# Performance work log

Measured on AMD Instinct MI355X. Metric: run time of the kernel, lower is better.

The kernel has to match this reference:

```python
import jax, jax.numpy as jnp
import numpy as np

EPS = 1.0


def _onedirectional_dist(a, b):
    # a: (B, M), b: (B, N) -> per-batch sum over M of min_n (a_m - b_n)^2
    d2 = (a[:, :, None] - b[:, None, :]) ** 2  # (B, M, N)
    return jnp.min(d2, axis=2).sum(axis=1)  # (B,)


def setup_inputs() -> dict:
    key = jax.random.key(0)
    k1, k2, k3 = jax.random.split(key, 3)
    target = jax.random.uniform(k1, (4, 240, 320), dtype=jnp.float32)
    bin_centers = jax.random.uniform(k2, (4, 256), dtype=jnp.float32)
    mask = jax.random.randint(k3, (4, 240, 320), 0, 2).astype(jnp.bool_)
    return {"target": target, "bin_centers": bin_centers, "mask": mask}


def reference(target, bin_centers, mask):
    # masked path of ChamferDistanceLoss.forward
    max_target = jnp.max(jnp.where(mask, target, -jnp.inf))
    max_center = jnp.max(bin_centers)
    mx = jnp.maximum(max_target, max_center)
    mn = jnp.minimum(max_target, max_center)
    pad_value = mx + (mx - mn) + EPS
    B = bin_centers.shape[0]
    # pad bin_centers with one extra column = pad_value
    mod_centers = jnp.concatenate(
        [bin_centers, jnp.broadcast_to(pad_value, (B, 1)).astype(bin_centers.dtype)],
        axis=1,
    )  # (B, n_bins + 1)
    # invalid target pixels replaced by pad_value
    mod_target = jnp.where(mask, target, pad_value).reshape(B, -1)  # (B, H*W)
    bidir = _onedirectional_dist(mod_centers, mod_target) + _onedirectional_dist(
        mod_target, mod_centers
    )
    return jnp.mean(bidir)
```

## Files before the change

### kernel.cpp

```cpp
#include <hip/hip_runtime.h>
#include <math.h>

#define B 4
#define HW 76800
#define NBINS 256
#define TPB 256
#define PXB 256
#define BPB (HW / PXB)


__global__ __launch_bounds__(256) void kmain(const float* __restrict__ target,
                                             const int* __restrict__ mask,
                                             const float* __restrict__ centers,
                                             float* __restrict__ out,
                                             float* __restrict__ part) {
    __shared__ __align__(16) float s_p[PXB];
    __shared__ __align__(16) float s_c[NBINS];
    __shared__ __align__(16) float s_c2[NBINS];
    __shared__ __align__(16) float s_d1[4][NBINS];
    __shared__ float s_red[4];
    const int tid = threadIdx.x;
    const int b   = blockIdx.y;
    const int blk = blockIdx.x;

    const int base = b * HW + blk * PXB;
    const float p = target[base + tid];
    const int   m = mask[base + tid];
    const float pm = m ? p : 1e18f;
    s_p[tid] = pm;
    {
        const float c = centers[b * NBINS + tid];
        s_c[tid]  = c;
        s_c2[tid] = c * c;
    }
    __syncthreads();

    const float q = p + p;
    float mnA = INFINITY, mnB = INFINITY;
    const float4* c4  = (const float4*)s_c;
    const float4* c24 = (const float4*)s_c2;
#pragma unroll 4
    for (int g = 0; g < NBINS / 8; ++g) {
        float4 ca = c4[2 * g],  cb = c4[2 * g + 1];
        float4 xa = c24[2 * g], xb = c24[2 * g + 1];
        float a0 = fmaf(-ca.x, q, xa.x), a1 = fmaf(-ca.y, q, xa.y);
        float a2 = fmaf(-ca.z, q, xa.z), a3 = fmaf(-ca.w, q, xa.w);
        mnA = fminf(mnA, fminf(fminf(a0, a1), fminf(a2, a3)));
        float b0 = fmaf(-cb.x, q, xb.x), b1 = fmaf(-cb.y, q, xb.y);
        float b2 = fmaf(-cb.z, q, xb.z), b3 = fmaf(-cb.w, q, xb.w);
        mnB = fminf(mnB, fminf(fminf(b0, b1), fminf(b2, b3)));
    }
    float acc = m ? fmaf(p, p, fminf(mnA, mnB)) : 0.f;

    const int w = tid >> 6, lane = tid & 63;
    const float4 cv = ((const float4*)s_c)[lane];
    float mk0 = INFINITY, mk1 = INFINITY, mk2 = INFINITY, mk3 = INFINITY;
    const float4* p4 = (const float4*)s_p;
#pragma unroll 8
    for (int j = 0; j < PXB / 4 / 4; ++j) {
        float4 pp = p4[w * 16 + j];
        float qx = pp.x + pp.x, sx = pp.x * pp.x;
        float qy = pp.y + pp.y, sy = pp.y * pp.y;
        float qz = pp.z + pp.z, sz = pp.z * pp.z;
        float qw = pp.w + pp.w, sw = pp.w * pp.w;
        float d0 = fmaf(-cv.x, qx, sx), d1 = fmaf(-cv.x, qy, sy);
        float d2 = fmaf(-cv.x, qz, sz), d3 = fmaf(-cv.x, qw, sw);
        mk0 = fminf(mk0, fminf(fminf(d0, d1), fminf(d2, d3)));
        float e0 = fmaf(-cv.y, qx, sx), e1 = fmaf(-cv.y, qy, sy);
        float e2 = fmaf(-cv.y, qz, sz), e3 = fmaf(-cv.y, qw, sw);
        mk1 = fminf(mk1, fminf(fminf(e0, e1), fminf(e2, e3)));
        float f0 = fmaf(-cv.z, qx, sx), f1 = fmaf(-cv.z, qy, sy);
        float f2 = fmaf(-cv.z, qz, sz), f3 = fmaf(-cv.z, qw, sw);
        mk2 = fminf(mk2, fminf(fminf(f0, f1), fminf(f2, f3)));
        float g0 = fmaf(-cv.w, qx, sx), g1 = fmaf(-cv.w, qy, sy);
        float g2 = fmaf(-cv.w, qz, sz), g3 = fmaf(-cv.w, qw, sw);
        mk3 = fminf(mk3, fminf(fminf(g0, g1), fminf(g2, g3)));
    }
    ((float4*)s_d1[w])[lane] = make_float4(mk0, mk1, mk2, mk3);

    for (int o = 32; o > 0; o >>= 1) acc += __shfl_down(acc, o);
    if (lane == 0) s_red[w] = acc;
    __syncthreads();

    float v = fminf(fminf(s_d1[0][tid], s_d1[1][tid]),
                    fminf(s_d1[2][tid], s_d1[3][tid]));
    part[(b * BPB + blk) * NBINS + tid] = v;

    if (tid == 0)
        atomicAdd(out, 0.25f * (s_red[0] + s_red[1] + s_red[2] + s_red[3]));
}

__global__ __launch_bounds__(256) void kfold(const float* __restrict__ centers,
                                             const float* __restrict__ part,
                                             float* __restrict__ out) {
    __shared__ float s_red[4];
    const int tid = threadIdx.x;
    const int b   = blockIdx.x;
    const float* pp = part + b * (BPB * NBINS) + tid;
    float m0 = INFINITY, m1 = INFINITY, m2 = INFINITY, m3 = INFINITY;
#pragma unroll 5
    for (int k = 0; k < BPB / 4; ++k) {
        m0 = fminf(m0, pp[(4 * k + 0) * NBINS]);
        m1 = fminf(m1, pp[(4 * k + 1) * NBINS]);
        m2 = fminf(m2, pp[(4 * k + 2) * NBINS]);
        m3 = fminf(m3, pp[(4 * k + 3) * NBINS]);
    }
    const float c = centers[b * NBINS + tid];
    float sum = fminf(fminf(m0, m1), fminf(m2, m3)) + c * c;
    for (int o = 32; o > 0; o >>= 1) sum += __shfl_down(sum, o);
    if ((tid & 63) == 0) s_red[tid >> 6] = sum;
    __syncthreads();
    if (tid == 0)
        atomicAdd(out, 0.25f * (s_red[0] + s_red[1] + s_red[2] + s_red[3]));
}

extern "C" void kernel_launch(void* const* d_in, const int* in_sizes, int n_in,
                              void* d_out, int out_size, void* d_ws, size_t ws_size,
                              hipStream_t stream) {
    const float* target  = (const float*)d_in[0];
    const float* centers = (const float*)d_in[1];
    const int*   mask    = (const int*)d_in[2];
    float* out  = (float*)d_out;
    float* part = (float*)d_ws;

    dim3 g(BPB, B);
    kmain<<<g, TPB, 0, stream>>>(target, mask, centers, out, part);
    kfold<<<dim3(B), TPB, 0, stream>>>(centers, part, out);
}
```

Baseline: 83.66 us.

## Drop LDS staging in main kernel and parallelize fold across bin groups

The main kernel no longer stages pixels and centers in shared memory with a barrier. It reads centers straight from global memory (uniform scalar loads) and re-reads target and mask per wave inside the center-side loop. The pixel-side min now uses the direct (c-p)^2 form instead of the expanded c^2-2cp form. The fold kernel is spread over 16 bin-groups per batch rather than one block per batch, giving more parallelism for the reduction of partial minima at the cost of more atomics.

```diff
diff --git a/kernel.cpp b/kernel.cpp
--- a/kernel.cpp
+++ b/kernel.cpp
@@ -7,6 +7,7 @@
 #define TPB 256
 #define PXB 256
 #define BPB (HW / PXB)
+#define FOLD_CB 16
 
 
 __global__ __launch_bounds__(256) void kmain(const float* __restrict__ target,
@@ -14,67 +15,54 @@
                                              const float* __restrict__ centers,
                                              float* __restrict__ out,
                                              float* __restrict__ part) {
-    __shared__ __align__(16) float s_p[PXB];
-    __shared__ __align__(16) float s_c[NBINS];
-    __shared__ __align__(16) float s_c2[NBINS];
     __shared__ __align__(16) float s_d1[4][NBINS];
     __shared__ float s_red[4];
-    const int tid = threadIdx.x;
-    const int b   = blockIdx.y;
-    const int blk = blockIdx.x;
+    const int tid  = threadIdx.x;
+    const int b    = blockIdx.y;
+    const int blk  = blockIdx.x;
+    const int lane = tid & 63;
+    const int w    = tid >> 6;
+    const int base = b * HW + blk * PXB;
 
-    const int base = b * HW + blk * PXB;
     const float p = target[base + tid];
     const int   m = mask[base + tid];
-    const float pm = m ? p : 1e18f;
-    s_p[tid] = pm;
-    {
-        const float c = centers[b * NBINS + tid];
-        s_c[tid]  = c;
-        s_c2[tid] = c * c;
-    }
-    __syncthreads();
+    const float4 cv = ((const float4*)(centers + b * NBINS))[lane];
 
-    const float q = p + p;
+    const float* __restrict__ cb = centers + b * NBINS;
     float mnA = INFINITY, mnB = INFINITY;
-    const float4* c4  = (const float4*)s_c;
-    const float4* c24 = (const float4*)s_c2;
 #pragma unroll 4
     for (int g = 0; g < NBINS / 8; ++g) {
-        float4 ca = c4[2 * g],  cb = c4[2 * g + 1];
-        float4 xa = c24[2 * g], xb = c24[2 * g + 1];
-        float a0 = fmaf(-ca.x, q, xa.x), a1 = fmaf(-ca.y, q, xa.y);
-        float a2 = fmaf(-ca.z, q, xa.z), a3 = fmaf(-ca.w, q, xa.w);
-        mnA = fminf(mnA, fminf(fminf(a0, a1), fminf(a2, a3)));
-        float b0 = fmaf(-cb.x, q, xb.x), b1 = fmaf(-cb.y, q, xb.y);
-        float b2 = fmaf(-cb.z, q, xb.z), b3 = fmaf(-cb.w, q, xb.w);
-        mnB = fminf(mnB, fminf(fminf(b0, b1), fminf(b2, b3)));
+        const float c0 = cb[8 * g + 0], c1 = cb[8 * g + 1];
+        const float c2 = cb[8 * g + 2], c3 = cb[8 * g + 3];
+        const float c4 = cb[8 * g + 4], c5 = cb[8 * g + 5];
+        const float c6 = cb[8 * g + 6], c7 = cb[8 * g + 7];
+        float t0 = c0 - p, t1 = c1 - p, t2 = c2 - p, t3 = c3 - p;
+        float t4 = c4 - p, t5 = c5 - p, t6 = c6 - p, t7 = c7 - p;
+        float d0 = t0 * t0, d1 = t1 * t1, d2 = t2 * t2, d3 = t3 * t3;
+        float d4 = t4 * t4, d5 = t5 * t5, d6 = t6 * t6, d7 = t7 * t7;
+        mnA = fminf(fminf(mnA, d3), fminf(fminf(d0, d1), d2));
+        mnB = fminf(fminf(mnB, d7), fminf(fminf(d4, d5), d6));
     }
-    float acc = m ? fmaf(p, p, fminf(mnA, mnB)) : 0.f;
+    float acc = m ? fminf(mnA, mnB) : 0.f;
 
-    const int w = tid >> 6, lane = tid & 63;
-    const float4 cv = ((const float4*)s_c)[lane];
+    const int wbase = base + __builtin_amdgcn_readfirstlane(w << 6);
     float mk0 = INFINITY, mk1 = INFINITY, mk2 = INFINITY, mk3 = INFINITY;
-    const float4* p4 = (const float4*)s_p;
-#pragma unroll 8
-    for (int j = 0; j < PXB / 4 / 4; ++j) {
-        float4 pp = p4[w * 16 + j];
-        float qx = pp.x + pp.x, sx = pp.x * pp.x;
-        float qy = pp.y + pp.y, sy = pp.y * pp.y;
-        float qz = pp.z + pp.z, sz = pp.z * pp.z;
-        float qw = pp.w + pp.w, sw = pp.w * pp.w;
-        float d0 = fmaf(-cv.x, qx, sx), d1 = fmaf(-cv.x, qy, sy);
-        float d2 = fmaf(-cv.x, qz, sz), d3 = fmaf(-cv.x, qw, sw);
-        mk0 = fminf(mk0, fminf(fminf(d0, d1), fminf(d2, d3)));
-        float e0 = fmaf(-cv.y, qx, sx), e1 = fmaf(-cv.y, qy, sy);
-        float e2 = fmaf(-cv.y, qz, sz), e3 = fmaf(-cv.y, qw, sw);
-        mk1 = fminf(mk1, fminf(fminf(e0, e1), fminf(e2, e3)));
-        float f0 = fmaf(-cv.z, qx, sx), f1 = fmaf(-cv.z, qy, sy);
-        float f2 = fmaf(-cv.z, qz, sz), f3 = fmaf(-cv.z, qw, sw);
-        mk2 = fminf(mk2, fminf(fminf(f0, f1), fminf(f2, f3)));
-        float g0 = fmaf(-cv.w, qx, sx), g1 = fmaf(-cv.w, qy, sy);
-        float g2 = fmaf(-cv.w, qz, sz), g3 = fmaf(-cv.w, qw, sw);
-        mk3 = fminf(mk3, fminf(fminf(g0, g1), fminf(g2, g3)));
+#pragma unroll 4
+    for (int j = 0; j < 64; j += 2) {
+        const float pa = target[wbase + j], pb = target[wbase + j + 1];
+        const int   ma = mask[wbase + j],   mb = mask[wbase + j + 1];
+        const float va = ma ? pa : 1e18f;
+        const float vb = mb ? pb : 1e18f;
+        float qa = va + va, sa = va * va;
+        float qb = vb + vb, sb = vb * vb;
+        float d0a = fmaf(-cv.x, qa, sa), d0b = fmaf(-cv.x, qb, sb);
+        float d1a = fmaf(-cv.y, qa, sa), d1b = fmaf(-cv.y, qb, sb);
+        float d2a = fmaf(-cv.z, qa, sa), d2b = fmaf(-cv.z, qb, sb);
+        float d3a = fmaf(-cv.w, qa, sa), d3b = fmaf(-cv.w, qb, sb);
+        mk0 = fminf(fminf(mk0, d0a), d0b);
+        mk1 = fminf(fminf(mk1, d1a), d1b);
+        mk2 = fminf(fminf(mk2, d2a), d2b);
+        mk3 = fminf(fminf(mk3, d3a), d3b);
     }
     ((float4*)s_d1[w])[lane] = make_float4(mk0, mk1, mk2, mk3);
 
@@ -93,25 +81,27 @@
 __global__ __launch_bounds__(256) void kfold(const float* __restrict__ centers,
                                              const float* __restrict__ part,
                                              float* __restrict__ out) {
-    __shared__ float s_red[4];
+    __shared__ float s_m[16][FOLD_CB];
     const int tid = threadIdx.x;
-    const int b   = blockIdx.x;
-    const float* pp = part + b * (BPB * NBINS) + tid;
-    float m0 = INFINITY, m1 = INFINITY, m2 = INFINITY, m3 = INFINITY;
-#pragma unroll 5
-    for (int k = 0; k < BPB / 4; ++k) {
-        m0 = fminf(m0, pp[(4 * k + 0) * NBINS]);
-        m1 = fminf(m1, pp[(4 * k + 1) * NBINS]);
-        m2 = fminf(m2, pp[(4 * k + 2) * NBINS]);
-        m3 = fminf(m3, pp[(4 * k + 3) * NBINS]);
+    const int b   = blockIdx.y;
+    const int cg  = blockIdx.x;
+    const int cc  = tid & 15;
+    const int kk  = tid >> 4;
+    const float* pp = part + b * (BPB * NBINS) + cg * FOLD_CB + cc;
+    float mn = INFINITY;
+    for (int j = kk; j < BPB; j += 16)
+        mn = fminf(mn, pp[j * NBINS]);
+    s_m[kk][cc] = mn;
+    __syncthreads();
+    if (tid < FOLD_CB) {
+        float m2 = INFINITY;
+#pragma unroll
+        for (int k = 0; k < 16; ++k) m2 = fminf(m2, s_m[k][tid]);
+        const float c = centers[b * NBINS + cg * FOLD_CB + tid];
+        float val = m2 + c * c;
+        for (int o = 8; o > 0; o >>= 1) val += __shfl_down(val, o);
+        if (tid == 0) atomicAdd(out, 0.25f * val);
     }
-    const float c = centers[b * NBINS + tid];
-    float sum = fminf(fminf(m0, m1), fminf(m2, m3)) + c * c;
-    for (int o = 32; o > 0; o >>= 1) sum += __shfl_down(sum, o);
-    if ((tid & 63) == 0) s_red[tid >> 6] = sum;
-    __syncthreads();
-    if (tid == 0)
-        atomicAdd(out, 0.25f * (s_red[0] + s_red[1] + s_red[2] + s_red[3]));
 }
 
 extern "C" void kernel_launch(void* const* d_in, const int* in_sizes, int n_in,
@@ -123,7 +113,8 @@
     float* out  = (float*)d_out;
     float* part = (float*)d_ws;
 
-    dim3 g(BPB, B);
-    kmain<<<g, TPB, 0, stream>>>(target, mask, centers, out, part);
-    kfold<<<dim3(B), TPB, 0, stream>>>(centers, part, out);
+    dim3 g1(BPB, B);
+    kmain<<<g1, TPB, 0, stream>>>(target, mask, centers, out, part);
+    dim3 g2(NBINS / FOLD_CB, B);
+    kfold<<<g2, TPB, 0, stream>>>(centers, part, out);
 }
```

After: 83.12 us. No clear change (-0.6%).
